# Kernel optimization log

Measured on AMD Instinct MI355X. Metric: run time of the kernel, lower is better.

The kernel has to match this reference:

```python
import jax, jax.numpy as jnp
import numpy as np

NUM_HEADS = 16


def setup_inputs() -> dict:
    key = jax.random.key(0)
    ks = jax.random.split(key, 7)
    dim, hd = 1024, 64
    B, H, W = 64, 14, 14  # B = batch * num_windows, 14x14 window
    x = jax.random.normal(ks[0], (B, H, W, dim), dtype=jnp.float32)
    qkv_w = jax.random.normal(ks[1], (dim, 3 * dim), dtype=jnp.float32) * (dim ** -0.5)
    qkv_b = jnp.zeros((3 * dim,), dtype=jnp.float32)
    proj_w = jax.random.normal(ks[2], (dim, dim), dtype=jnp.float32) * (dim ** -0.5)
    proj_b = jnp.zeros((dim,), dtype=jnp.float32)
    rel_pos_h = jax.random.normal(ks[3], (2 * H - 1, hd), dtype=jnp.float32) * 0.02
    rel_pos_w = jax.random.normal(ks[4], (2 * W - 1, hd), dtype=jnp.float32) * 0.02
    return {"x": x, "qkv_w": qkv_w, "qkv_b": qkv_b, "proj_w": proj_w,
            "proj_b": proj_b, "rel_pos_h": rel_pos_h, "rel_pos_w": rel_pos_w}


def reference(x, qkv_w, qkv_b, proj_w, proj_b, rel_pos_h, rel_pos_w):
    B, H, W, dim = x.shape
    nH = NUM_HEADS
    hd = dim // nH
    scale = hd ** -0.5

    # qkv projection: [B, HW, 3*dim]
    qkv = x.reshape(B, H * W, dim) @ qkv_w + qkv_b
    # -> [3, nH, B, HW, hd] -> [3, nH*B, HW, hd]
    qkv = qkv.reshape(B, H * W, 3, nH, hd).transpose(2, 3, 0, 1, 4)
    qkv = qkv.reshape(3, nH * B, H * W, hd)
    q, k, v = qkv[0], qkv[1], qkv[2]

    # scaled QK^T: [nH*B, HW, HW]
    attn = jnp.einsum('bqc,bkc->bqk', q * scale, k)

    # decomposed relative position bias (q_size == k_size, no interpolation)
    Rh = rel_pos_h[jnp.arange(H)[:, None] - jnp.arange(H)[None, :] + (H - 1)]  # [H,H,hd]
    Rw = rel_pos_w[jnp.arange(W)[:, None] - jnp.arange(W)[None, :] + (W - 1)]  # [W,W,hd]
    r_q = q.reshape(nH * B, H, W, hd)
    rel_h = jnp.einsum('bhwc,hkc->bhwk', r_q, Rh)  # [nH*B,H,W,H]
    rel_w = jnp.einsum('bhwc,wkc->bhwk', r_q, Rw)  # [nH*B,H,W,W]
    attn = (attn.reshape(nH * B, H, W, H, W)
            + rel_h[:, :, :, :, None]
            + rel_w[:, :, :, None, :]).reshape(nH * B, H * W, H * W)

    attn = jax.nn.softmax(attn, axis=-1)
    out = attn @ v  # [nH*B, HW, hd]

    # merge heads: [nH,B,H,W,hd] -> [B,H,W,dim]
    out = out.reshape(nH, B, H, W, hd).transpose(1, 2, 3, 0, 4).reshape(B, H, W, dim)
    return out @ proj_w + proj_b
```

## Files before the change

kernel.cpp:

```cpp
#include <hip/hip_runtime.h>
#include <cstdint>
#include <cstddef>

typedef unsigned short u16;
typedef unsigned int u32;
typedef float f32x4 __attribute__((ext_vector_type(4)));
typedef short short8 __attribute__((ext_vector_type(8)));
typedef u32 u32x2 __attribute__((ext_vector_type(2)));

#define HW 196
#define DIM 1024
#define HD 64
#define SP 208
#define SPV 224
#define NBH 1024

__device__ __forceinline__ float bf2f(u16 x){
  union { u32 u; float f; } c; c.u = ((u32)x) << 16; return c.f;
}
__device__ __forceinline__ u16 f2bf(float f){
  union { float f; u32 u; } c; c.f = f;
  return (u16)((c.u + 0x7fffu + ((c.u >> 16) & 1u)) >> 16);
}
__device__ __forceinline__ u32 cvtpk_bf16(float lo, float hi){
  u32 r;
  asm("v_cvt_pk_bf16_f32 %0, %1, %2" : "=v"(r) : "v"(lo), "v"(hi));
  return r;
}
#define LGKM_FENCE() do { \
    asm volatile("s_waitcnt lgkmcnt(0)" ::: "memory"); \
    __builtin_amdgcn_sched_barrier(0); \
  } while (0)
#define DS_FENCE() do { \
    asm volatile("s_waitcnt lgkmcnt(0)" ::: "memory"); \
    __builtin_amdgcn_sched_barrier(0x7F); \
  } while (0)
#define WAITV0() asm volatile("s_waitcnt vmcnt(0)" ::: "memory")
#define BAR() __builtin_amdgcn_s_barrier()

typedef __attribute__((address_space(3))) void lds_void_t;
typedef __attribute__((address_space(1))) const void glb_void_t;
__device__ __forceinline__ void gload_lds16(const void* g, void* l){
  __builtin_amdgcn_global_load_lds((glb_void_t*)g, (lds_void_t*)l, 16, 0, 0);
}

__global__ __launch_bounds__(256) void k_xcvt(const float* __restrict__ x,
                                              u16* __restrict__ xb, int n8){
  int i = blockIdx.x * 256 + threadIdx.x;
  if (i < n8){
    const f32x4* p = (const f32x4*)(x + (size_t)i * 8);
    f32x4 v0 = p[0], v1 = p[1];
    short8 t;
    #pragma unroll
    for (int e = 0; e < 4; ++e){
      t[e]   = (short)f2bf(v0[e]);
      t[4+e] = (short)f2bf(v1[e]);
    }
    *(short8*)(xb + (size_t)i * 8) = t;
  }
}

__global__ __launch_bounds__(256) void k_rprep(const float* __restrict__ rph,
                                               const float* __restrict__ rpw,
                                               u16* __restrict__ rphb,
                                               u16* __restrict__ rpwb){
  int r = threadIdx.x >> 3, cc = (threadIdx.x & 7) * 8;
  #pragma unroll
  for (int t = 0; t < 2; ++t){
    const float* src = t ? rpw : rph;
    u16* dst = t ? rpwb : rphb;
    short8 v;
    #pragma unroll
    for (int e = 0; e < 8; ++e)
      v[e] = (r < 27) ? (short)f2bf(src[(size_t)r * 64 + cc + e]) : (short)0;
    *(short8*)(dst + (size_t)r * 64 + cc) = v;
  }
}

__global__ __launch_bounds__(256) void k_wT(const float* __restrict__ w,
                                            u16* __restrict__ wT, int K, int N){
  __shared__ float t[32][33];
  int n0 = blockIdx.x * 32, k0 = blockIdx.y * 32;
  int c = threadIdx.x & 31, rr = threadIdx.x >> 5;
  #pragma unroll
  for (int i = 0; i < 4; ++i){
    int r = rr + i*8;
    t[r][c] = w[(size_t)(k0 + r) * N + n0 + c];
  }
  __syncthreads();
  #pragma unroll
  for (int i = 0; i < 4; ++i){
    int r = rr + i*8;
    wT[(size_t)(n0 + r) * K + k0 + c] = f2bf(t[c][r]);
  }
}

template<int MODE>
__global__ __launch_bounds__(512, 2) void k_g256(const u16* __restrict__ Ab,
    const u16* __restrict__ Bt, const float* __restrict__ bias,
    u16* __restrict__ qg, u16* __restrict__ kg, u16* __restrict__ vTg,
    float* __restrict__ outf, int K, int N, int ntm, int ntn)
{
  extern __shared__ __align__(16) u16 smem[];
  const int tid = threadIdx.x;
  const int lane = tid & 63, wv = tid >> 6;
  const int wr = wv >> 2, wc = wv & 3;
  const int l16 = lane & 15, lk = lane >> 4;

  const int nwg = ntm * ntn;
  int bid = blockIdx.x;
  int q8 = nwg >> 3, r8 = nwg & 7;
  int xcd = bid & 7, loc = bid >> 3;
  int wgid = (xcd < r8 ? xcd*(q8+1) : r8*(q8+1) + (xcd - r8)*q8) + loc;
  int gsz = 8 * ntn;
  int g = wgid / gsz, rem = wgid - g * gsz;
  int gm = ntm - g * 8; if (gm > 8) gm = 8;
  int ry = g * 8 + rem % gm;
  int cy = rem / gm;
  const size_t m0 = (size_t)ry * 256;
  const size_t n0 = (size_t)cy * 256;
  const int nk = K >> 5;

  auto off = [&](int d, int ab){ return (d*2 + ab) * 8192; };

  auto stageH = [&](int d, int ab, int tile){
    const u16* src = ab ? Bt : Ab;
    size_t rb = ab ? n0 : m0;
    int c = (lane & 3) ^ ((lane >> 3) & 3);
    #pragma unroll
    for (int i = 0; i < 2; ++i){
      int rh = 32*wv + 16*i + (lane >> 2);
      gload_lds16(src + (rb + rh) * (size_t)K + tile*32 + c*8,
                  smem + off(d, ab) + (32*wv + 16*i) * 32);
    }
  };
  auto ldA = [&](short8* a, int d, int h){
    #pragma unroll
    for (int m2 = 0; m2 < 4; ++m2){
      int r = wr*128 + h*64 + m2*16 + l16;
      a[m2] = *(const short8*)(smem + off(d,0) + r*32 + ((lk ^ ((r>>1)&3)) << 3));
    }
  };
  auto ldB = [&](short8* b, int d){
    #pragma unroll
    for (int ni = 0; ni < 4; ++ni){
      int r = wc*64 + ni*16 + l16;
      b[ni] = *(const short8*)(smem + off(d,1) + r*32 + ((lk ^ ((r>>1)&3)) << 3));
    }
  };

  f32x4 acc[8][4] = {};
  auto mm = [&](int h, short8* a, short8* b){
    __builtin_amdgcn_s_setprio(1);
    #pragma unroll
    for (int m2 = 0; m2 < 4; ++m2)
      #pragma unroll
      for (int ni = 0; ni < 4; ++ni)
        acc[h*4+m2][ni] = __builtin_amdgcn_mfma_f32_16x16x32_bf16(b[ni], a[m2], acc[h*4+m2][ni], 0, 0, 0);
    __builtin_amdgcn_s_setprio(0);
  };

  stageH(0, 0, 0); stageH(0, 1, 0);
  WAITV0(); BAR();

  #pragma unroll 1
  for (int kt = 0; kt < nk; ++kt){
    const int d = kt & 1, dn = d ^ 1;
    const int tn = (kt + 1 < nk) ? kt + 1 : nk - 1;
    short8 a[4], b[4];
    ldA(a, d, 0); ldB(b, d);
    stageH(dn, 0, tn); stageH(dn, 1, tn);
    BAR(); LGKM_FENCE();
    mm(0, a, b);
    BAR();
    ldA(a, d, 1);
    LGKM_FENCE();
    mm(1, a, b);
    WAITV0();
    BAR();
  }

  const int rowb = (int)m0 + wr*128;
  const int colb = (int)n0 + wc*64;
  if constexpr (MODE == 1){
    #pragma unroll
    for (int mi = 0; mi < 8; ++mi){
      int r = rowb + mi*16 + l16;
      float* orow = outf + (size_t)r * N;
      #pragma unroll
      for (int ni = 0; ni < 4; ++ni){
        int c0 = colb + ni*16 + lk*4;
        f32x4 bz = *(const f32x4*)(bias + c0);
        f32x4 v = acc[mi][ni] + bz;
        *(f32x4*)(orow + c0) = v;
      }
    }
  } else {
    const int t3 = colb >> 10;
    if (t3 < 2){
      u16* dst0 = (t3 == 0) ? qg : kg;
      const float sc = (t3 == 0) ? 1.0f : 0.125f;
      #pragma unroll
      for (int mi = 0; mi < 8; ++mi){
        int r = rowb + mi*16 + l16;
        int b = r / 196, n = r - b * 196;
        #pragma unroll
        for (int ni = 0; ni < 4; ++ni){
          int rr2 = ((colb & 1023) + ni*16);
          int hh = rr2 >> 6, ccb = (rr2 & 63) + lk*4;
          const float* bz = bias + colb + ni*16 + lk*4;
          u32 w0 = cvtpk_bf16((acc[mi][ni][0] + bz[0])*sc, (acc[mi][ni][1] + bz[1])*sc);
          u32 w1 = cvtpk_bf16((acc[mi][ni][2] + bz[2])*sc, (acc[mi][ni][3] + bz[3])*sc);
          u32* dst = (u32*)(dst0 + ((size_t)(hh*64 + b) * SP + n) * HD + ccb);
          dst[0] = w0; dst[1] = w1;
        }
      }
    } else {
      #pragma unroll
      for (int mi = 0; mi < 8; ++mi){
        int r = rowb + mi*16 + l16;
        int b = r / 196, n = r - b * 196;
        #pragma unroll
        for (int ni = 0; ni < 4; ++ni){
          int col0 = colb + ni*16 + lk*4;
          f32x4 bz = *(const f32x4*)(bias + col0);
          int rem2 = col0 & 1023;
          int hh = rem2 >> 6, cc0 = rem2 & 63;
          u16* base = vTg + ((size_t)(hh*64 + b) * HD + cc0) * SPV + n;
          #pragma unroll
          for (int i = 0; i < 4; ++i)
            base[(size_t)i * SPV] = f2bf(acc[mi][ni][i] + bz[i]);
        }
      }
    }
  }
}

#define KSTR 144
#define VSTR 464
#define PWB  7424
__global__ __launch_bounds__(832, 1) void k_attn(
    const u16* __restrict__ qg, const u16* __restrict__ kg, const u16* __restrict__ vTg,
    const u16* __restrict__ rphb, const u16* __restrict__ rpwb,
    u16* __restrict__ ao)
{
  extern __shared__ __align__(16) char asmem[];
  char* Klds = asmem;
  char* Vlds = asmem + 29952;
  const int tid = threadIdx.x, lane = tid & 63, wvi = tid >> 6;
  const int l16 = lane & 15, lk = lane >> 4;
  char*  wbase = asmem + 59648 + wvi * PWB;
  float* relT  = (float*)wbase;
  u32*   Pp    = (u32*)wbase;

  const int bh = blockIdx.x;
  const int hh = bh >> 6, bb = bh & 63;
  const u16* qb = qg  + (size_t)bh * SP * HD;
  const u16* kb = kg  + (size_t)bh * SP * HD;
  const u16* vb = vTg + (size_t)bh * HD * SPV;

  for (int c = tid; c < 1664; c += 832){
    int row = c >> 3, colb = (c & 7) << 4;
    short8 d = *(const short8*)((const char*)kb + row*128 + colb);
    *(short8*)(Klds + row*KSTR + colb) = d;
  }
  for (int c = tid; c < 1792; c += 832){
    int row = c / 28, colb = (c - row*28) << 4;
    short8 d = *(const short8*)((const char*)vb + row*448 + colb);
    *(short8*)(Vlds + row*VSTR + colb) = d;
  }
  __syncthreads();

  const int mt = wvi;
  const short8 a0 = *(const short8*)(qb + (size_t)(mt*16 + l16) * HD + lk*8);
  const short8 a1 = *(const short8*)(qb + (size_t)(mt*16 + l16) * HD + 32 + lk*8);

  {
    f32x4 z = {0.f,0.f,0.f,0.f};
    f32x4 racc[2][2] = {{z,z},{z,z}};
    #pragma unroll
    for (int dt = 0; dt < 2; ++dt){
      short8 h0 = *(const short8*)(rphb + (size_t)(dt*16 + l16) * 64 + lk*8);
      short8 h1 = *(const short8*)(rphb + (size_t)(dt*16 + l16) * 64 + 32 + lk*8);
      short8 w0 = *(const short8*)(rpwb + (size_t)(dt*16 + l16) * 64 + lk*8);
      short8 w1 = *(const short8*)(rpwb + (size_t)(dt*16 + l16) * 64 + 32 + lk*8);
      racc[0][dt] = __builtin_amdgcn_mfma_f32_16x16x32_bf16(h0, a0, racc[0][dt], 0, 0, 0);
      racc[0][dt] = __builtin_amdgcn_mfma_f32_16x16x32_bf16(h1, a1, racc[0][dt], 0, 0, 0);
      racc[1][dt] = __builtin_amdgcn_mfma_f32_16x16x32_bf16(w0, a0, racc[1][dt], 0, 0, 0);
      racc[1][dt] = __builtin_amdgcn_mfma_f32_16x16x32_bf16(w1, a1, racc[1][dt], 0, 0, 0);
    }
    #pragma unroll
    for (int t = 0; t < 2; ++t)
      #pragma unroll
      for (int dt = 0; dt < 2; ++dt)
        *(f32x4*)(relT + l16*68 + t*32 + dt*16 + lk*4) = racc[t][dt];
  }
  DS_FENCE();

  int qr = mt*16 + l16;
  int qrc = qr > HW-1 ? HW-1 : qr;
  int qh = qrc / 14, qw = qrc - 14*qh;
  const float* rrow = relT + l16*68;
  const int dh0 = qh + 13, dw0 = 32 + qw + 13;
  const int lk4 = lk*4;

  f32x4 sacc[13];
  #pragma unroll
  for (int nt = 0; nt < 13; ++nt){
    #pragma unroll
    for (int i = 0; i < 4; ++i){
      int k = nt*16 + lk4 + i;
      int kh = (k * 4682) >> 16;
      if (nt == 12 && kh > 13) kh = 13;
      int kw = k - kh*14;
      float bias = rrow[dh0 - kh] + rrow[dw0 - kw];
      sacc[nt][i] = (nt == 12 && lk != 0) ? -1e30f : bias;
    }
  }

  #pragma unroll
  for (int nt = 0; nt < 13; ++nt){
    int row = nt*16 + l16;
    short8 b0 = *(const short8*)(Klds + row*KSTR + lk*16);
    short8 b1 = *(const short8*)(Klds + row*KSTR + 64 + lk*16);
    sacc[nt] = __builtin_amdgcn_mfma_f32_16x16x32_bf16(b0, a0, sacc[nt], 0, 0, 0);
    sacc[nt] = __builtin_amdgcn_mfma_f32_16x16x32_bf16(b1, a1, sacc[nt], 0, 0, 0);
  }

  float m;
  {
    float t0[13];
    #pragma unroll
    for (int nt = 0; nt < 13; ++nt)
      t0[nt] = fmaxf(fmaxf(sacc[nt][0], sacc[nt][1]), fmaxf(sacc[nt][2], sacc[nt][3]));
    float a01 = fmaxf(t0[0], t0[1]),  a23 = fmaxf(t0[2], t0[3]);
    float a45 = fmaxf(t0[4], t0[5]),  a67 = fmaxf(t0[6], t0[7]);
    float a89 = fmaxf(t0[8], t0[9]),  aab = fmaxf(t0[10], t0[11]);
    m = fmaxf(fmaxf(fmaxf(a01, a23), fmaxf(a45, a67)), fmaxf(fmaxf(a89, aab), t0[12]));
  }
  m = fmaxf(m, __shfl_xor(m, 16, 64));
  m = fmaxf(m, __shfl_xor(m, 32, 64));
  float sum;
  {
    float s4[13];
    #pragma unroll
    for (int nt = 0; nt < 13; ++nt){
      #pragma unroll
      for (int i = 0; i < 4; ++i)
        sacc[nt][i] = __expf(sacc[nt][i] - m);
      s4[nt] = (sacc[nt][0] + sacc[nt][1]) + (sacc[nt][2] + sacc[nt][3]);
    }
    float b01 = s4[0]+s4[1], b23 = s4[2]+s4[3], b45 = s4[4]+s4[5];
    float b67 = s4[6]+s4[7], b89 = s4[8]+s4[9], bab = s4[10]+s4[11];
    sum = ((b01+b23) + (b45+b67)) + ((b89+bab) + s4[12]);
  }
  sum += __shfl_xor(sum, 16, 64);
  sum += __shfl_xor(sum, 32, 64);
  float inv = 1.0f / sum;

  DS_FENCE();
  u32* prow = Pp + l16*116;
  #pragma unroll
  for (int nt = 0; nt < 13; ++nt){
    u32x2 wpk;
    wpk[0] = cvtpk_bf16(sacc[nt][0], sacc[nt][1]);
    wpk[1] = cvtpk_bf16(sacc[nt][2], sacc[nt][3]);
    *(u32x2*)(prow + nt*8 + lk*2) = wpk;
  }
  { u32x2 zz = {0u, 0u}; *(u32x2*)(prow + 104 + lk*2) = zz; }
  DS_FENCE();

  f32x4 z = {0.f,0.f,0.f,0.f};
  f32x4 oacc[4] = {z,z,z,z};
  #pragma unroll
  for (int kt = 0; kt < 7; ++kt){
    short8 pa = *(const short8*)(prow + kt*16 + lk4);
    #pragma unroll
    for (int dt = 0; dt < 4; ++dt){
      short8 bv = *(const short8*)(Vlds + (dt*16 + l16)*VSTR + kt*64 + lk*16);
      oacc[dt] = __builtin_amdgcn_mfma_f32_16x16x32_bf16(bv, pa, oacc[dt], 0, 0, 0);
    }
  }
  int qrow = mt*16 + l16;
  if (qrow < HW){
    u16* orow = ao + ((size_t)bb * HW + qrow) * DIM + hh * HD;
    #pragma unroll
    for (int dt = 0; dt < 4; ++dt){
      u32 lo = cvtpk_bf16(oacc[dt][0]*inv, oacc[dt][1]*inv);
      u32 hi = cvtpk_bf16(oacc[dt][2]*inv, oacc[dt][3]*inv);
      u32* dst = (u32*)(orow + dt*16 + lk4);
      dst[0] = lo; dst[1] = hi;
    }
  }
}

extern "C" void kernel_launch(void* const* d_in, const int* in_sizes, int n_in,
                              void* d_out, int out_size, void* d_ws, size_t ws_size,
                              hipStream_t stream)
{
  const float* x      = (const float*)d_in[0];
  const float* qkv_w  = (const float*)d_in[1];
  const float* qkv_b  = (const float*)d_in[2];
  const float* proj_w = (const float*)d_in[3];
  const float* proj_b = (const float*)d_in[4];
  const float* rph    = (const float*)d_in[5];
  const float* rpw    = (const float*)d_in[6];
  float* out = (float*)d_out;
  char* ws = (char*)d_ws;

  size_t off = 0;
  auto alloc = [&](size_t b){ size_t r = off; off += (b + 255) & ~(size_t)255; return r; };
  u16* wqkvT = (u16*)(ws + alloc((size_t)3072*1024*2));
  u16* wprojT= (u16*)(ws + alloc((size_t)1024*1024*2));
  u16* qg    = (u16*)(ws + alloc((size_t)NBH*SP*HD*2));
  u16* kg    = (u16*)(ws + alloc((size_t)NBH*SP*HD*2));
  u16* vTg   = (u16*)(ws + alloc((size_t)NBH*HD*SPV*2));
  u16* rphb  = (u16*)(ws + alloc((size_t)32*64*2));
  u16* rpwb  = (u16*)(ws + alloc((size_t)32*64*2));
  u16* xb    = (u16*)(ws + alloc((size_t)12544*1024*2));
  u16* ao    = xb;

  hipFuncSetAttribute((const void*)k_g256<0>, hipFuncAttributeMaxDynamicSharedMemorySize, 65536);
  hipFuncSetAttribute((const void*)k_g256<1>, hipFuncAttributeMaxDynamicSharedMemorySize, 65536);
  hipFuncSetAttribute((const void*)k_attn,    hipFuncAttributeMaxDynamicSharedMemorySize, 156160);

  hipMemsetAsync(vTg, 0, (size_t)NBH*HD*SPV*2, stream);

  k_xcvt<<<(12544*1024/8 + 255)/256, 256, 0, stream>>>(x, xb, 12544*1024/8);
  k_wT<<<dim3(96, 32), 256, 0, stream>>>(qkv_w, wqkvT, 1024, 3072);
  k_wT<<<dim3(32, 32), 256, 0, stream>>>(proj_w, wprojT, 1024, 1024);
  k_rprep<<<1, 256, 0, stream>>>(rph, rpw, rphb, rpwb);

  k_g256<0><<<49*12, 512, 65536, stream>>>(xb, wqkvT, qkv_b, qg, kg, vTg, nullptr,
                                           1024, 3072, 49, 12);
  k_attn<<<1024, 832, 156160, stream>>>(qg, kg, vTg, rphb, rpwb, ao);
  k_g256<1><<<49*4, 512, 65536, stream>>>(ao, wprojT, proj_b, nullptr, nullptr, nullptr, out,
                                          1024, 1024, 49, 4);
}
```

Measured before the change: 236.4 us.

## Fuse prep kernels into one launch and simplify GEMM main-loop synchronization

Merges the x conversion, both weight transposes and the rel-pos conversion into a single kernel that dispatches on block index, which removes three launches. Separately, the GEMM main loop drops the explicit barriers, lgkm waits and setprio calls in favour of one __syncthreads per iteration. That relaxes the hand-tuned interleaving of LDS reads, async global-to-LDS loads and MFMA. It could expose LDS load latency or races on the double buffer, since the compiler now has to order the async loads on its own.

```diff
diff --git a/kernel.cpp b/kernel.cpp
--- a/kernel.cpp
+++ b/kernel.cpp
@@ -27,16 +27,10 @@
   asm("v_cvt_pk_bf16_f32 %0, %1, %2" : "=v"(r) : "v"(lo), "v"(hi));
   return r;
 }
-#define LGKM_FENCE() do { \
-    asm volatile("s_waitcnt lgkmcnt(0)" ::: "memory"); \
-    __builtin_amdgcn_sched_barrier(0); \
-  } while (0)
 #define DS_FENCE() do { \
     asm volatile("s_waitcnt lgkmcnt(0)" ::: "memory"); \
     __builtin_amdgcn_sched_barrier(0x7F); \
   } while (0)
-#define WAITV0() asm volatile("s_waitcnt vmcnt(0)" ::: "memory")
-#define BAR() __builtin_amdgcn_s_barrier()
 
 typedef __attribute__((address_space(3))) void lds_void_t;
 typedef __attribute__((address_space(1))) const void glb_void_t;
@@ -44,54 +38,56 @@
   __builtin_amdgcn_global_load_lds((glb_void_t*)g, (lds_void_t*)l, 16, 0, 0);
 }
 
-__global__ __launch_bounds__(256) void k_xcvt(const float* __restrict__ x,
-                                              u16* __restrict__ xb, int n8){
-  int i = blockIdx.x * 256 + threadIdx.x;
-  if (i < n8){
+__global__ __launch_bounds__(256) void k_prep(const float* __restrict__ x,
+    u16* __restrict__ xb,
+    const float* __restrict__ qkv_w, u16* __restrict__ wqkvT,
+    const float* __restrict__ proj_w, u16* __restrict__ wprojT,
+    const float* __restrict__ rph, const float* __restrict__ rpw,
+    u16* __restrict__ rphb, u16* __restrict__ rpwb)
+{
+  __shared__ float t[32][33];
+  int blk = blockIdx.x;
+  if (blk < 6272){
+    int i = blk * 256 + threadIdx.x;
     const f32x4* p = (const f32x4*)(x + (size_t)i * 8);
     f32x4 v0 = p[0], v1 = p[1];
-    short8 t;
+    short8 tt;
     #pragma unroll
     for (int e = 0; e < 4; ++e){
-      t[e]   = (short)f2bf(v0[e]);
-      t[4+e] = (short)f2bf(v1[e]);
-    }
-    *(short8*)(xb + (size_t)i * 8) = t;
-  }
-}
-
-__global__ __launch_bounds__(256) void k_rprep(const float* __restrict__ rph,
-                                               const float* __restrict__ rpw,
-                                               u16* __restrict__ rphb,
-                                               u16* __restrict__ rpwb){
-  int r = threadIdx.x >> 3, cc = (threadIdx.x & 7) * 8;
-  #pragma unroll
-  for (int t = 0; t < 2; ++t){
-    const float* src = t ? rpw : rph;
-    u16* dst = t ? rpwb : rphb;
-    short8 v;
-    #pragma unroll
-    for (int e = 0; e < 8; ++e)
-      v[e] = (r < 27) ? (short)f2bf(src[(size_t)r * 64 + cc + e]) : (short)0;
-    *(short8*)(dst + (size_t)r * 64 + cc) = v;
-  }
-}
-
-__global__ __launch_bounds__(256) void k_wT(const float* __restrict__ w,
-                                            u16* __restrict__ wT, int K, int N){
-  __shared__ float t[32][33];
-  int n0 = blockIdx.x * 32, k0 = blockIdx.y * 32;
-  int c = threadIdx.x & 31, rr = threadIdx.x >> 5;
-  #pragma unroll
-  for (int i = 0; i < 4; ++i){
-    int r = rr + i*8;
-    t[r][c] = w[(size_t)(k0 + r) * N + n0 + c];
-  }
-  __syncthreads();
-  #pragma unroll
-  for (int i = 0; i < 4; ++i){
-    int r = rr + i*8;
-    wT[(size_t)(n0 + r) * K + k0 + c] = f2bf(t[c][r]);
+      tt[e]   = (short)f2bf(v0[e]);
+      tt[4+e] = (short)f2bf(v1[e]);
+    }
+    *(short8*)(xb + (size_t)i * 8) = tt;
+  } else if (blk < 10368){
+    const float* w; u16* wT; int K = 1024, N; int idx;
+    if (blk < 9344){ w = qkv_w; wT = wqkvT; N = 3072; idx = blk - 6272; }
+    else           { w = proj_w; wT = wprojT; N = 1024; idx = blk - 9344; }
+    int nb = N >> 5;
+    int n0 = (idx % nb) * 32, k0 = (idx / nb) * 32;
+    int c = threadIdx.x & 31, rr = threadIdx.x >> 5;
+    #pragma unroll
+    for (int i = 0; i < 4; ++i){
+      int r = rr + i*8;
+      t[r][c] = w[(size_t)(k0 + r) * N + n0 + c];
+    }
+    __syncthreads();
+    #pragma unroll
+    for (int i = 0; i < 4; ++i){
+      int r = rr + i*8;
+      wT[(size_t)(n0 + r) * K + k0 + c] = f2bf(t[c][r]);
+    }
+  } else {
+    int r = threadIdx.x >> 3, cc = (threadIdx.x & 7) * 8;
+    #pragma unroll
+    for (int tsel = 0; tsel < 2; ++tsel){
+      const float* src = tsel ? rpw : rph;
+      u16* dst = tsel ? rpwb : rphb;
+      short8 v;
+      #pragma unroll
+      for (int e = 0; e < 8; ++e)
+        v[e] = (r < 27) ? (short)f2bf(src[(size_t)r * 64 + cc + e]) : (short)0;
+      *(short8*)(dst + (size_t)r * 64 + cc) = v;
+    }
   }
 }
 
@@ -151,17 +147,15 @@
 
   f32x4 acc[8][4] = {};
   auto mm = [&](int h, short8* a, short8* b){
-    __builtin_amdgcn_s_setprio(1);
     #pragma unroll
     for (int m2 = 0; m2 < 4; ++m2)
       #pragma unroll
       for (int ni = 0; ni < 4; ++ni)
         acc[h*4+m2][ni] = __builtin_amdgcn_mfma_f32_16x16x32_bf16(b[ni], a[m2], acc[h*4+m2][ni], 0, 0, 0);
-    __builtin_amdgcn_s_setprio(0);
   };
 
   stageH(0, 0, 0); stageH(0, 1, 0);
-  WAITV0(); BAR();
+  __syncthreads();
 
   #pragma unroll 1
   for (int kt = 0; kt < nk; ++kt){
@@ -170,14 +164,10 @@
     short8 a[4], b[4];
     ldA(a, d, 0); ldB(b, d);
     stageH(dn, 0, tn); stageH(dn, 1, tn);
-    BAR(); LGKM_FENCE();
     mm(0, a, b);
-    BAR();
     ldA(a, d, 1);
-    LGKM_FENCE();
     mm(1, a, b);
-    WAITV0();
-    BAR();
+    __syncthreads();
   }
 
   const int rowb = (int)m0 + wr*128;
@@ -426,11 +416,8 @@
 
   hipMemsetAsync(vTg, 0, (size_t)NBH*HD*SPV*2, stream);
 
-  k_xcvt<<<(12544*1024/8 + 255)/256, 256, 0, stream>>>(x, xb, 12544*1024/8);
-  k_wT<<<dim3(96, 32), 256, 0, stream>>>(qkv_w, wqkvT, 1024, 3072);
-  k_wT<<<dim3(32, 32), 256, 0, stream>>>(proj_w, wprojT, 1024, 1024);
-  k_rprep<<<1, 256, 0, stream>>>(rph, rpw, rphb, rpwb);
-
+  k_prep<<<10369, 256, 0, stream>>>(x, xb, qkv_w, wqkvT, proj_w, wprojT,
+                                    rph, rpw, rphb, rpwb);
   k_g256<0><<<49*12, 512, 65536, stream>>>(xb, wqkvT, qkv_b, qg, kg, vTg, nullptr,
                                            1024, 3072, 49, 12);
   k_attn<<<1024, 832, 156160, stream>>>(qg, kg, vTg, rphb, rpwb, ao);
```

Measured after the change: 237.8 us. Within noise of the previous version (+0.6%).
